# Kernel tuning notes

Measured on AMD Instinct MI355X. Metric: run time of the kernel, lower is better.

## Reference

```python
import jax, jax.numpy as jnp
import numpy as np

BATCH = 1024
NUM_GENES = 20000          # output_dimension == cfg['num_genes']
NONGENE_DIM = 64           # input_dimension - output_dimension
EMB_DIM = 32               # cfg['gene_embedding_size']
INPUT_DIM = NUM_GENES + NONGENE_DIM
FC_IN = NONGENE_DIM + 1 + EMB_DIM  # concat(nongene, x_j, emb_j)


def setup_inputs() -> dict:
    key = jax.random.key(0)
    k1, k2, k3, k4 = jax.random.split(key, 4)
    x = jax.random.normal(k1, (BATCH, INPUT_DIM), dtype=jnp.float32)
    # nn.Embedding default init: N(0,1)
    emb = jax.random.normal(k2, (NUM_GENES, EMB_DIM), dtype=jnp.float32)
    # nn.Linear(FC_IN, 1): weight [1, FC_IN] U(-1/sqrt(in), 1/sqrt(in)); flatten to [FC_IN]
    bound = 1.0 / np.sqrt(FC_IN)
    W = jax.random.uniform(k3, (FC_IN,), dtype=jnp.float32, minval=-bound, maxval=bound)
    b = jax.random.uniform(k4, (), dtype=jnp.float32, minval=-bound, maxval=bound)
    return {"x": x, "emb": emb, "W": W, "b": b}


def reference(x, emb, W, b):
    # Original loop: y[:, j] = fc(concat(nongene, x[:, j:j+1], emb[j].repeat(B,1)))
    # fc weight splits into [W_ng | w_x | W_e]; the linear is separable:
    #   y[b, j] = nongene[b] . W_ng + x[b, j] * w_x + emb[j] . W_e + bias
    G, E = emb.shape
    D_ng = W.shape[0] - 1 - E
    nongene = x[:, -D_ng:]                       # [B, D_ng]
    W_ng, w_x, W_e = W[:D_ng], W[D_ng], W[D_ng + 1:]
    ng_term = nongene @ W_ng                     # [B]  constant across genes
    gene_term = emb @ W_e                        # [G]  constant across batch
    y = ng_term[:, None] + x[:, :G] * w_x + gene_term[None, :] + b  # [B, G]
    return y
```

## Files before the change

### kernel.cpp

```cpp
#include <hip/hip_runtime.h>

#define BATCH 1024
#define NUM_GENES 20000
#define NONGENE_DIM 64
#define EMB_DIM 32
#define INPUT_DIM (NUM_GENES + NONGENE_DIM)
#define G4 (NUM_GENES / 4)
#define ROWS_PER_BLOCK 4

#define GENE_THREADS (NUM_GENES * 8)
#define NG_THREADS   (BATCH * 16)
#define PRE_TOTAL    (GENE_THREADS + NG_THREADS)

__global__ __launch_bounds__(256)
void dlge_precompute(const float* __restrict__ x,
                     const float* __restrict__ emb,
                     const float* __restrict__ W,
                     const float* __restrict__ bptr,
                     float* __restrict__ ws) {
    const int tid = blockIdx.x * blockDim.x + threadIdx.x;

    if (tid < GENE_THREADS) {
        const int g = tid >> 3;
        const int k = tid & 7;
        const float4 e = reinterpret_cast<const float4*>(emb)[g * (EMB_DIM / 4) + k];
        float p = e.x * W[NONGENE_DIM + 1 + 4 * k + 0]
                + e.y * W[NONGENE_DIM + 1 + 4 * k + 1]
                + e.z * W[NONGENE_DIM + 1 + 4 * k + 2]
                + e.w * W[NONGENE_DIM + 1 + 4 * k + 3];
        p += __shfl_down(p, 4, 8);
        p += __shfl_down(p, 2, 8);
        p += __shfl_down(p, 1, 8);
        if (k == 0) ws[g] = p;
    } else if (tid < PRE_TOTAL) {
        const int t   = tid - GENE_THREADS;
        const int row = t >> 4;
        const int k   = t & 15;
        const float4 v = reinterpret_cast<const float4*>(
            x + (size_t)row * INPUT_DIM + NUM_GENES)[k];
        float p = v.x * W[4 * k + 0] + v.y * W[4 * k + 1]
                + v.z * W[4 * k + 2] + v.w * W[4 * k + 3];
        p += __shfl_down(p, 8, 16);
        p += __shfl_down(p, 4, 16);
        p += __shfl_down(p, 2, 16);
        p += __shfl_down(p, 1, 16);
        if (k == 0) ws[NUM_GENES + row] = p + bptr[0];
    }
}

__global__ __launch_bounds__(256)
void dlge_main(const float* __restrict__ x,
               const float* __restrict__ ws,
               const float* __restrict__ W,
               float* __restrict__ y) {
    const int j = blockIdx.x * 256 + threadIdx.x;
    if (j >= G4) return;
    const int row0 = blockIdx.y * ROWS_PER_BLOCK;

    const float wx = W[NONGENE_DIM];
    const float4 g4 = reinterpret_cast<const float4*>(ws)[j];

    float s[ROWS_PER_BLOCK];
#pragma unroll
    for (int r = 0; r < ROWS_PER_BLOCK; ++r)
        s[r] = ws[NUM_GENES + row0 + r];

    float4 x4[ROWS_PER_BLOCK];
#pragma unroll
    for (int r = 0; r < ROWS_PER_BLOCK; ++r)
        x4[r] = reinterpret_cast<const float4*>(
            x + (size_t)(row0 + r) * INPUT_DIM)[j];

#pragma unroll
    for (int r = 0; r < ROWS_PER_BLOCK; ++r) {
        float4 o;
        o.x = s[r] + x4[r].x * wx + g4.x;
        o.y = s[r] + x4[r].y * wx + g4.y;
        o.z = s[r] + x4[r].z * wx + g4.z;
        o.w = s[r] + x4[r].w * wx + g4.w;
        reinterpret_cast<float4*>(y + (size_t)(row0 + r) * NUM_GENES)[j] = o;
    }
}

extern "C" void kernel_launch(void* const* d_in, const int* in_sizes, int n_in,
                              void* d_out, int out_size, void* d_ws, size_t ws_size,
                              hipStream_t stream) {
    const float* x   = (const float*)d_in[0];
    const float* emb = (const float*)d_in[1];
    const float* W   = (const float*)d_in[2];
    const float* b   = (const float*)d_in[3];
    float* y  = (float*)d_out;
    float* ws = (float*)d_ws;

    dlge_precompute<<<PRE_TOTAL / 256, 256, 0, stream>>>(x, emb, W, b, ws);

    dim3 grid((G4 + 255) / 256, BATCH / ROWS_PER_BLOCK);
    dlge_main<<<grid, 256, 0, stream>>>(x, ws, W, y);
}
```

Before: 34.63 us.

## Use persistent grid-stride main kernel with software-prefetched loads

Replaces the 2D grid (4 rows per block) with a fixed 2048-block grid-stride kernel over flattened float4 elements. Each thread handles 10 elements and loads the next element's x, gene term and row scalar before computing and storing the current one. This is meant to keep more memory requests in flight and cut block-launch overhead on a bandwidth-bound elementwise pass. The cost is a per-element integer division to recover row and column, and fewer independent loads per thread than the previous 4-row unroll.

```diff
diff --git a/kernel.cpp b/kernel.cpp
--- a/kernel.cpp
+++ b/kernel.cpp
@@ -6,7 +6,7 @@
 #define EMB_DIM 32
 #define INPUT_DIM (NUM_GENES + NONGENE_DIM)
 #define G4 (NUM_GENES / 4)
-#define ROWS_PER_BLOCK 4
+#define IN4 (INPUT_DIM / 4)
 
 #define GENE_THREADS (NUM_GENES * 8)
 #define NG_THREADS   (BATCH * 16)
@@ -48,37 +48,60 @@
     }
 }
 
-__global__ __launch_bounds__(256)
+#define F4_TOTAL   (BATCH * G4)
+#define MAIN_BLOCKS 2048
+#define STRIDE     (MAIN_BLOCKS * 256)
+#define N_ITER     10
+
+__global__ __launch_bounds__(256, 8)
 void dlge_main(const float* __restrict__ x,
                const float* __restrict__ ws,
                const float* __restrict__ W,
                float* __restrict__ y) {
-    const int j = blockIdx.x * 256 + threadIdx.x;
-    if (j >= G4) return;
-    const int row0 = blockIdx.y * ROWS_PER_BLOCK;
+    const float wx = W[NONGENE_DIM];
+    const float4* __restrict__ xf4  = reinterpret_cast<const float4*>(x);
+    const float4* __restrict__ gtf4 = reinterpret_cast<const float4*>(ws);
+    float4* __restrict__ yf4        = reinterpret_cast<float4*>(y);
 
-    const float wx = W[NONGENE_DIM];
-    const float4 g4 = reinterpret_cast<const float4*>(ws)[j];
+    int idx = blockIdx.x * 256 + threadIdx.x;
 
-    float s[ROWS_PER_BLOCK];
-#pragma unroll
-    for (int r = 0; r < ROWS_PER_BLOCK; ++r)
-        s[r] = ws[NUM_GENES + row0 + r];
+    unsigned row = (unsigned)idx / (unsigned)G4;
+    int      col = idx - (int)row * G4;
+    float4   xv  = xf4[(size_t)row * IN4 + col];
+    float4   gv  = gtf4[col];
+    float    sv  = ws[NUM_GENES + row];
 
-    float4 x4[ROWS_PER_BLOCK];
-#pragma unroll
-    for (int r = 0; r < ROWS_PER_BLOCK; ++r)
-        x4[r] = reinterpret_cast<const float4*>(
-            x + (size_t)(row0 + r) * INPUT_DIM)[j];
+    for (int i = 0; i < N_ITER - 1; ++i) {
+        const int  nidx = idx + STRIDE;
+        const bool nv   = (nidx < F4_TOTAL);
+        unsigned nrow = 0; int ncol = 0;
+        float4 nxv = {0.f, 0.f, 0.f, 0.f};
+        float4 ngv = {0.f, 0.f, 0.f, 0.f};
+        float  nsv = 0.f;
+        if (nv) {
+            nrow = (unsigned)nidx / (unsigned)G4;
+            ncol = nidx - (int)nrow * G4;
+            nxv  = xf4[(size_t)nrow * IN4 + ncol];
+            ngv  = gtf4[ncol];
+            nsv  = ws[NUM_GENES + nrow];
+        }
+        float4 o;
+        o.x = sv + xv.x * wx + gv.x;
+        o.y = sv + xv.y * wx + gv.y;
+        o.z = sv + xv.z * wx + gv.z;
+        o.w = sv + xv.w * wx + gv.w;
+        yf4[(size_t)row * G4 + col] = o;
 
-#pragma unroll
-    for (int r = 0; r < ROWS_PER_BLOCK; ++r) {
+        idx = nidx; row = nrow; col = ncol; xv = nxv; gv = ngv; sv = nsv;
+    }
+
+    if (idx < F4_TOTAL) {
         float4 o;
-        o.x = s[r] + x4[r].x * wx + g4.x;
-        o.y = s[r] + x4[r].y * wx + g4.y;
-        o.z = s[r] + x4[r].z * wx + g4.z;
-        o.w = s[r] + x4[r].w * wx + g4.w;
-        reinterpret_cast<float4*>(y + (size_t)(row0 + r) * NUM_GENES)[j] = o;
+        o.x = sv + xv.x * wx + gv.x;
+        o.y = sv + xv.y * wx + gv.y;
+        o.z = sv + xv.z * wx + gv.z;
+        o.w = sv + xv.w * wx + gv.w;
+        yf4[(size_t)row * G4 + col] = o;
     }
 }
 
@@ -93,7 +116,5 @@
     float* ws = (float*)d_ws;
 
     dlge_precompute<<<PRE_TOTAL / 256, 256, 0, stream>>>(x, emb, W, b, ws);
-
-    dim3 grid((G4 + 255) / 256, BATCH / ROWS_PER_BLOCK);
-    dlge_main<<<grid, 256, 0, stream>>>(x, ws, W, y);
+    dlge_main<<<MAIN_BLOCKS, 256, 0, stream>>>(x, ws, W, y);
 }
```

Result: no change. 34.78 us (+0.4%).
